# Kernel tuning notes

Measured on AMD Instinct MI355X. Metric: run time of the kernel, lower is better.

The kernel has to match this reference:

```python
import jax, jax.numpy as jnp
import numpy as np

N_NODES = 100000
N_EDGES = 1600000
D = 128


def setup_inputs() -> dict:
    key = jax.random.key(0)
    k1, k2, k3, k4 = jax.random.split(key, 4)
    x = jax.random.normal(k1, (N_NODES, D), dtype=jnp.float32)
    edge_index = jax.random.randint(k2, (2, N_EDGES), 0, N_NODES, dtype=jnp.int32)
    # torch.nn.Linear(nfeat, nclass): weight [out, in], bias [out]
    W = jax.random.normal(k3, (D, D), dtype=jnp.float32) * (1.0 / np.sqrt(D))
    b = jax.random.normal(k4, (D,), dtype=jnp.float32) * 0.01
    return {"x": x, "edge_index": edge_index, "W": W, "b": b}


def reference(x, edge_index, W, b):
    n = x.shape[0]
    # gcn_norm: add self-loops, edge_weight = 1
    loop = jnp.arange(n, dtype=edge_index.dtype)
    row = jnp.concatenate([edge_index[0], loop])  # source
    col = jnp.concatenate([edge_index[1], loop])  # target
    deg = jax.ops.segment_sum(jnp.ones_like(col, dtype=x.dtype), col, num_segments=n)
    dinv = jnp.where(deg > 0, deg ** -0.5, 0.0)
    norm = dinv[row] * dinv[col]  # [E+N]
    # K=1 propagate: out[col] += norm * x[row]
    agg = jax.ops.segment_sum(x[row] * norm[:, None], col, num_segments=n)
    # linear (y = agg @ W^T + b), then relu + residual
    h = agg @ W.T + b
    return x + jax.nn.relu(h)
```

## Files before the change

### kernel.cpp

```cpp
#include <hip/hip_runtime.h>

#define NN 100000
#define NE 1600000
#define DD 128
#define NBLK 98
#define NBUK 782
#define NB_AC 256
#define CHUNK 6250
#define SCAN_N (NBUK * NB_AC)
#define NB_SCAN 196

typedef __attribute__((ext_vector_type(8))) short bf16x8;
typedef __attribute__((ext_vector_type(4))) float f32x4;
typedef __attribute__((ext_vector_type(2))) float f32x2;

__device__ __forceinline__ float bf2f(unsigned short u) {
    return __uint_as_float(((unsigned)u) << 16);
}
__device__ __forceinline__ unsigned short f2bf(float f) {
    unsigned u = __float_as_uint(f);
    u += 0x7FFFu + ((u >> 16) & 1u);
    return (unsigned short)(u >> 16);
}

__global__ __launch_bounds__(256) void k_hist(const int* __restrict__ col,
                                              unsigned* __restrict__ part) {
    __shared__ unsigned hist[NBUK];
    int t = threadIdx.x, blk = blockIdx.x;
    for (int i = t; i < NBUK; i += 256) hist[i] = 0;
    __syncthreads();
    int beg = blk * CHUNK, end = beg + CHUNK;
    for (int e = beg + t; e < end; e += 256)
        atomicAdd(&hist[col[e] >> 7], 1u);
    __syncthreads();
    for (int i = t; i < NBUK; i += 256)
        part[(size_t)i * NB_AC + blk] = hist[i];
}

__global__ __launch_bounds__(1024) void k_bsum(const unsigned* __restrict__ part,
                                               unsigned* __restrict__ sb) {
    __shared__ unsigned red[1024];
    int t = threadIdx.x;
    int i = blockIdx.x * 1024 + t;
    red[t] = i < SCAN_N ? part[i] : 0;
    __syncthreads();
    for (int off = 512; off > 0; off >>= 1) {
        if (t < off) red[t] += red[t + off];
        __syncthreads();
    }
    if (t == 0) sb[blockIdx.x] = red[0];
}

__global__ __launch_bounds__(1024) void k_scanpart(const unsigned* __restrict__ part,
                                                   const unsigned* __restrict__ sb,
                                                   unsigned* __restrict__ off) {
    __shared__ unsigned s2[256];
    __shared__ unsigned s[1024];
    int t = threadIdx.x;
    if (t < 256) s2[t] = (t < NB_SCAN) ? sb[t] : 0;
    __syncthreads();
    for (int o = 1; o < 256; o <<= 1) {
        unsigned v = 0;
        if (t < 256 && t >= o) v = s2[t - o];
        __syncthreads();
        if (t < 256) s2[t] += v;
        __syncthreads();
    }
    unsigned boff = blockIdx.x == 0 ? 0 : s2[blockIdx.x - 1];
    int i = blockIdx.x * 1024 + t;
    unsigned v = i < SCAN_N ? part[i] : 0;
    s[t] = v;
    __syncthreads();
    for (int o = 1; o < 1024; o <<= 1) {
        unsigned u = t >= o ? s[t - o] : 0;
        __syncthreads();
        s[t] += u;
        __syncthreads();
    }
    if (i < SCAN_N) off[i] = boff + s[t] - v;
}

__global__ __launch_bounds__(256) void k_scatter_pk(const int* __restrict__ row,
                                                    const int* __restrict__ col,
                                                    const unsigned* __restrict__ off,
                                                    unsigned* __restrict__ packed) {
    __shared__ unsigned cur[NBUK];
    int t = threadIdx.x, blk = blockIdx.x;
    for (int i = t; i < NBUK; i += 256) cur[i] = off[(size_t)i * NB_AC + blk];
    __syncthreads();
    int beg = blk * CHUNK, end = beg + CHUNK;
    for (int e = beg + t; e < end; e += 256) {
        int c = col[e];
        unsigned pos = atomicAdd(&cur[c >> 7], 1u);
        packed[pos] = ((unsigned)(c & 127) << 17) | (unsigned)row[e];
    }
}

__global__ __launch_bounds__(256) void k_bucket_csr(const unsigned* __restrict__ off,
                                                    const unsigned* __restrict__ packed,
                                                    float* __restrict__ dinv,
                                                    int* __restrict__ rowptr,
                                                    int* __restrict__ esrc) {
    __shared__ unsigned deg[128], pre[128], tmp[128];
    int t = threadIdx.x;
    int buk = blockIdx.x;
    unsigned bstart = off[(size_t)buk * NB_AC];
    unsigned bend = (buk == NBUK - 1) ? (unsigned)NE : off[(size_t)(buk + 1) * NB_AC];
    if (t < 128) deg[t] = 0;
    __syncthreads();
    for (unsigned e = bstart + t; e < bend; e += 256)
        atomicAdd(&deg[packed[e] >> 17], 1u);
    __syncthreads();
    if (t < 128) tmp[t] = deg[t];
    __syncthreads();
    for (int o = 1; o < 128; o <<= 1) {
        unsigned v = 0;
        if (t < 128 && t >= o) v = tmp[t - o];
        __syncthreads();
        if (t < 128) tmp[t] += v;
        __syncthreads();
    }
    if (t < 128) {
        pre[t] = tmp[t] - deg[t];
        int n = buk * 128 + t;
        if (n < NN) {
            dinv[n] = 1.0f / sqrtf((float)(deg[t] + 1));
            rowptr[n] = (int)(bstart + pre[t]);
        }
    }
    if (buk == NBUK - 1 && t == 0) rowptr[NN] = NE;
    __syncthreads();
    if (t < 128) deg[t] = pre[t];
    __syncthreads();
    for (unsigned e = bstart + t; e < bend; e += 256) {
        unsigned p = packed[e];
        unsigned pos = atomicAdd(&deg[p >> 17], 1u);
        esrc[bstart + pos] = (int)(p & 0x1FFFFu);
    }
}

__global__ void k_wb(const float* __restrict__ W, unsigned short* __restrict__ wbs) {
    int unit = blockIdx.x * 256 + threadIdx.x;
    int row = unit >> 4;
    int c0 = (unit & 15) * 8;
    float4 v0 = *(const float4*)(W + row * DD + c0);
    float4 v1 = *(const float4*)(W + row * DD + c0 + 4);
    bf16x8 h;
    h[0] = (short)f2bf(v0.x); h[1] = (short)f2bf(v0.y);
    h[2] = (short)f2bf(v0.z); h[3] = (short)f2bf(v0.w);
    h[4] = (short)f2bf(v1.x); h[5] = (short)f2bf(v1.y);
    h[6] = (short)f2bf(v1.z); h[7] = (short)f2bf(v1.w);
    int byte = (row * 256 + c0 * 2) ^ ((row & 7) << 4);
    *(bf16x8*)((char*)wbs + byte) = h;
}

__global__ __launch_bounds__(256) void k_ygemm(const float* __restrict__ x,
                                               const unsigned short* __restrict__ wbs,
                                               const float* __restrict__ dinv,
                                               unsigned char* __restrict__ yb8) {
    __shared__ unsigned short wb[DD * DD];
    int t = threadIdx.x;
#pragma unroll
    for (int i = 0; i < 8; ++i)
        ((float4*)wb)[t + 256 * i] = ((const float4*)wbs)[t + 256 * i];
    __syncthreads();

    int wave = t >> 6;
    int lane = t & 63;
    int lrow = lane & 15;
    int kg = lane >> 4;

    int arow = blockIdx.x * 64 + wave * 16 + lrow;
    int arc = arow < NN ? arow : NN - 1;
    bf16x8 afrag[4];
#pragma unroll
    for (int ks = 0; ks < 4; ++ks) {
        const float* src = x + (size_t)arc * DD + ks * 32 + kg * 8;
        float4 v0 = *(const float4*)src;
        float4 v1 = *(const float4*)(src + 4);
        bf16x8 h;
        h[0] = (short)f2bf(v0.x); h[1] = (short)f2bf(v0.y);
        h[2] = (short)f2bf(v0.z); h[3] = (short)f2bf(v0.w);
        h[4] = (short)f2bf(v1.x); h[5] = (short)f2bf(v1.y);
        h[6] = (short)f2bf(v1.z); h[7] = (short)f2bf(v1.w);
        afrag[ks] = h;
    }

    f32x4 acc[8];
#pragma unroll
    for (int ct = 0; ct < 8; ++ct) acc[ct] = (f32x4)(0.f);

#pragma unroll
    for (int ct = 0; ct < 8; ++ct) {
        int wrow = ct * 16 + lrow;
#pragma unroll
        for (int ks = 0; ks < 4; ++ks) {
            int byte = (wrow * 256 + ks * 64 + kg * 16) ^ ((wrow & 7) << 4);
            bf16x8 bfrag = *(const bf16x8*)((char*)wb + byte);
            acc[ct] = __builtin_amdgcn_mfma_f32_16x16x32_bf16(afrag[ks], bfrag, acc[ct], 0, 0, 0);
        }
    }

#pragma unroll
    for (int j = 0; j < 4; ++j) {
        int m = blockIdx.x * 64 + wave * 16 + kg * 4 + j;
        if (m < NN) {
            float s = dinv[m];
            unsigned w0 = 0, w1 = 0;
            w0 = __builtin_amdgcn_cvt_pk_fp8_f32(s * acc[0][j], s * acc[1][j], w0, false);
            w0 = __builtin_amdgcn_cvt_pk_fp8_f32(s * acc[2][j], s * acc[3][j], w0, true);
            w1 = __builtin_amdgcn_cvt_pk_fp8_f32(s * acc[4][j], s * acc[5][j], w1, false);
            w1 = __builtin_amdgcn_cvt_pk_fp8_f32(s * acc[6][j], s * acc[7][j], w1, true);
            uint2 o; o.x = w0; o.y = w1;
            *(uint2*)(yb8 + (size_t)m * DD + lrow * 8) = o;
        }
    }
}

__global__ __launch_bounds__(256) void k_gather_fp8(const int* __restrict__ rowptr,
                                                    const int* __restrict__ esrc,
                                                    const unsigned char* __restrict__ yb8,
                                                    const float* __restrict__ x,
                                                    const float* __restrict__ dinv,
                                                    const float* __restrict__ bias,
                                                    float* __restrict__ out) {
    int t = threadIdx.x;
    int gl = t & 31;
    int node = blockIdx.x * 8 + (t >> 5);
    if (node >= NN) return;
    int beg = rowptr[node];
    int end = rowptr[node + 1];
    float dc = dinv[node];

    unsigned su = *(const unsigned*)(yb8 + (size_t)node * DD + gl * 4);
    f32x2 a01 = __builtin_amdgcn_cvt_pk_f32_fp8(su, false);
    f32x2 a23 = __builtin_amdgcn_cvt_pk_f32_fp8(su, true);

    int e = beg;
    for (; e + 7 < end; e += 8) {
        unsigned uu[8];
#pragma unroll
        for (int u = 0; u < 8; ++u) {
            int r = esrc[e + u];
            uu[u] = *(const unsigned*)(yb8 + (size_t)r * DD + gl * 4);
        }
#pragma unroll
        for (int u = 0; u < 8; ++u) {
            a01 += __builtin_amdgcn_cvt_pk_f32_fp8(uu[u], false);
            a23 += __builtin_amdgcn_cvt_pk_f32_fp8(uu[u], true);
        }
    }
    for (; e < end; ++e) {
        int r = esrc[e];
        unsigned u = *(const unsigned*)(yb8 + (size_t)r * DD + gl * 4);
        a01 += __builtin_amdgcn_cvt_pk_f32_fp8(u, false);
        a23 += __builtin_amdgcn_cvt_pk_f32_fp8(u, true);
    }

    float vals[4] = {a01.x, a01.y, a23.x, a23.y};
    int q = gl >> 1;
    int c0 = (gl & 1) * 4;
#pragma unroll
    for (int i = 0; i < 4; ++i) {
        int n = (c0 + i) * 16 + q;
        float h = dc * vals[i] + bias[n];
        out[(size_t)node * DD + n] = x[(size_t)node * DD + n] + fmaxf(h, 0.f);
    }
}

__global__ void k_count(const int* __restrict__ col, int* __restrict__ deg) {
    int i = blockIdx.x * blockDim.x + threadIdx.x;
    if (i < NE) atomicAdd(&deg[col[i]], 1);
}
__global__ __launch_bounds__(1024) void k_blocksum_dinv(const int* __restrict__ deg,
                                                        int* __restrict__ bsum,
                                                        float* __restrict__ dinv) {
    __shared__ int red[1024];
    int t = threadIdx.x;
    int i = blockIdx.x * 1024 + t;
    int d = i < NN ? deg[i] : 0;
    if (i < NN) dinv[i] = 1.0f / sqrtf((float)(d + 1));
    red[t] = d;
    __syncthreads();
    for (int off = 512; off > 0; off >>= 1) {
        if (t < off) red[t] += red[t + off];
        __syncthreads();
    }
    if (t == 0) bsum[blockIdx.x] = red[0];
}
__global__ void k_scanbsum(const int* __restrict__ bsum, int* __restrict__ boff) {
    __shared__ int s[128];
    int t = threadIdx.x;
    s[t] = t < NBLK ? bsum[t] : 0;
    __syncthreads();
    for (int off = 1; off < 128; off <<= 1) {
        int v = t >= off ? s[t - off] : 0;
        __syncthreads();
        s[t] += v;
        __syncthreads();
    }
    if (t < NBLK) boff[t] = (t == 0) ? 0 : s[t - 1];
}
__global__ __launch_bounds__(1024) void k_scanwrite(const int* __restrict__ deg,
                                                    const int* __restrict__ boff,
                                                    int* __restrict__ rowptr) {
    __shared__ int s[1024];
    int t = threadIdx.x;
    int i = blockIdx.x * 1024 + t;
    int v = i < NN ? deg[i] : 0;
    s[t] = v;
    __syncthreads();
    for (int off = 1; off < 1024; off <<= 1) {
        int u = t >= off ? s[t - off] : 0;
        __syncthreads();
        s[t] += u;
        __syncthreads();
    }
    if (i < NN) rowptr[i] = boff[blockIdx.x] + s[t] - v;
    if (i == 0) rowptr[NN] = NE;
}
__global__ void k_fill(const int* __restrict__ row, const int* __restrict__ col,
                       const int* __restrict__ rowptr, int* __restrict__ cnt,
                       int* __restrict__ esrc) {
    int i = blockIdx.x * blockDim.x + threadIdx.x;
    if (i < NE) {
        int c = col[i];
        int pos = rowptr[c] + atomicAdd(&cnt[c], 1);
        esrc[pos] = row[i];
    }
}
__global__ __launch_bounds__(256) void k_gather(const int* __restrict__ rowptr,
                                                const int* __restrict__ esrc,
                                                const float* __restrict__ x,
                                                const float* __restrict__ dinv,
                                                float* __restrict__ agg) {
    int t = threadIdx.x;
    int lane = t & 31;
    int node = blockIdx.x * 8 + (t >> 5);
    if (node >= NN) return;
    int beg = rowptr[node];
    int end = rowptr[node + 1];
    float dc = dinv[node];
    float4 xv = ((const float4*)(x + (size_t)node * DD))[lane];
    float4 acc;
    acc.x = dc * xv.x; acc.y = dc * xv.y; acc.z = dc * xv.z; acc.w = dc * xv.w;
    int e = beg;
    for (; e + 1 < end; e += 2) {
        int r0 = esrc[e];
        int r1 = esrc[e + 1];
        float s0 = dinv[r0];
        float s1 = dinv[r1];
        float4 v0 = ((const float4*)(x + (size_t)r0 * DD))[lane];
        float4 v1 = ((const float4*)(x + (size_t)r1 * DD))[lane];
        acc.x += s0 * v0.x + s1 * v1.x;
        acc.y += s0 * v0.y + s1 * v1.y;
        acc.z += s0 * v0.z + s1 * v1.z;
        acc.w += s0 * v0.w + s1 * v1.w;
    }
    if (e < end) {
        int r = esrc[e];
        float s = dinv[r];
        float4 v = ((const float4*)(x + (size_t)r * DD))[lane];
        acc.x += s * v.x; acc.y += s * v.y; acc.z += s * v.z; acc.w += s * v.w;
    }
    acc.x *= dc; acc.y *= dc; acc.z *= dc; acc.w *= dc;
    ((float4*)(agg + (size_t)node * DD))[lane] = acc;
}
__global__ void k_transpose_w(const float* __restrict__ W, float* __restrict__ Wt) {
    int c = blockIdx.x;
    int k = threadIdx.x;
    Wt[k * DD + c] = W[c * DD + k];
}
__global__ __launch_bounds__(256) void k_gemm(const float* __restrict__ x,
                                              const float* __restrict__ Wt,
                                              const float* __restrict__ bias,
                                              float* __restrict__ out) {
    __shared__ float wt[DD * DD];
    int t = threadIdx.x;
    for (int i = t; i < DD * DD / 4; i += 256)
        ((float4*)wt)[i] = ((const float4*)Wt)[i];
    __syncthreads();

    int grp = t >> 5;
    int c4  = (t & 31) * 4;
    int rbase = blockIdx.x * 64 + grp * 8;

    float acc[8][4];
#pragma unroll
    for (int i = 0; i < 8; i++)
#pragma unroll
        for (int j = 0; j < 4; j++) acc[i][j] = 0.0f;

    for (int k = 0; k < DD; k += 4) {
        float4 w0 = *(const float4*)&wt[(k + 0) * DD + c4];
        float4 w1 = *(const float4*)&wt[(k + 1) * DD + c4];
        float4 w2 = *(const float4*)&wt[(k + 2) * DD + c4];
        float4 w3 = *(const float4*)&wt[(k + 3) * DD + c4];
#pragma unroll
        for (int i = 0; i < 8; i++) {
            int rr = rbase + i;
            rr = rr < NN ? rr : NN - 1;
            float4 a = *(const float4*)&out[(size_t)rr * DD + k];
            acc[i][0] += a.x * w0.x + a.y * w1.x + a.z * w2.x + a.w * w3.x;
            acc[i][1] += a.x * w0.y + a.y * w1.y + a.z * w2.y + a.w * w3.y;
            acc[i][2] += a.x * w0.z + a.y * w1.z + a.z * w2.z + a.w * w3.z;
            acc[i][3] += a.x * w0.w + a.y * w1.w + a.z * w2.w + a.w * w3.w;
        }
    }

    float4 bv = *(const float4*)&bias[c4];
#pragma unroll
    for (int i = 0; i < 8; i++) {
        int r = rbase + i;
        if (r < NN) {
            float4 xv = *(const float4*)&x[(size_t)r * DD + c4];
            float4 o;
            o.x = xv.x + fmaxf(acc[i][0] + bv.x, 0.0f);
            o.y = xv.y + fmaxf(acc[i][1] + bv.y, 0.0f);
            o.z = xv.z + fmaxf(acc[i][2] + bv.z, 0.0f);
            o.w = xv.w + fmaxf(acc[i][3] + bv.w, 0.0f);
            *(float4*)&out[(size_t)r * DD + c4] = o;
        }
    }
}

extern "C" void kernel_launch(void* const* d_in, const int* in_sizes, int n_in,
                              void* d_out, int out_size, void* d_ws, size_t ws_size,
                              hipStream_t stream) {
    const float* x   = (const float*)d_in[0];
    const int*   ei  = (const int*)d_in[1];
    const float* W   = (const float*)d_in[2];
    const float* b   = (const float*)d_in[3];
    const int* row = ei;
    const int* col = ei + NE;

    float* out = (float*)d_out;

    char* ws = (char*)d_ws;
    unsigned* part   = (unsigned*)ws;
    unsigned* off    = (unsigned*)(ws + 800768);
    unsigned* sb     = (unsigned*)(ws + 1601536);
    float*    dinv   = (float*)(ws + 1602352);
    int*      rowptr = (int*)(ws + 2002352);
    unsigned* packed = (unsigned*)(ws + 2402368);
    unsigned short* wbs = (unsigned short*)(ws + 8802368);
    float*    Wt     = (float*)(ws + 8802368);
    int*      esrc   = (int*)(ws + 8867904);
    unsigned char* yb8 = (unsigned char*)(ws + 15267904);

    bool big_ws = ws_size >= 28100000;

    if (big_ws) {
        k_hist<<<NB_AC, 256, 0, stream>>>(col, part);
        k_bsum<<<NB_SCAN, 1024, 0, stream>>>(part, sb);
        k_scanpart<<<NB_SCAN, 1024, 0, stream>>>(part, sb, off);
        k_scatter_pk<<<NB_AC, 256, 0, stream>>>(row, col, off, packed);
        k_bucket_csr<<<NBUK, 256, 0, stream>>>(off, packed, dinv, rowptr, esrc);
        k_wb<<<8, 256, 0, stream>>>(W, wbs);
        k_ygemm<<<(NN + 63) / 64, 256, 0, stream>>>(x, wbs, dinv, yb8);
        k_gather_fp8<<<(NN + 7) / 8, 256, 0, stream>>>(rowptr, esrc, yb8, x, dinv, b, out);
    } else {
        int* cnt  = (int*)ws;
        int* bsum = (int*)(ws + 1601536);
        int* boff = (int*)(ws + 400000);
        hipMemsetAsync(cnt, 0, NN * sizeof(int), stream);
        k_count<<<(NE + 255) / 256, 256, 0, stream>>>(col, cnt);
        k_blocksum_dinv<<<NBLK, 1024, 0, stream>>>(cnt, bsum, dinv);
        k_scanbsum<<<1, 128, 0, stream>>>(bsum, boff);
        k_scanwrite<<<NBLK, 1024, 0, stream>>>(cnt, boff, rowptr);
        hipMemsetAsync(cnt, 0, NN * sizeof(int), stream);
        k_fill<<<(NE + 255) / 256, 256, 0, stream>>>(row, col, rowptr, cnt, esrc);
        k_gather<<<(NN + 7) / 8, 256, 0, stream>>>(rowptr, esrc, x, dinv, out);
        k_transpose_w<<<DD, DD, 0, stream>>>(W, Wt);
        k_gemm<<<(NN + 63) / 64, 256, 0, stream>>>(x, Wt, b, out);
    }
}
```

Before: 135.0 us.

## Split fp8 features into column planes and gather in four cache-sized passes

The GEMM now writes its fp8 output as four column planes of 32 bytes per node instead of one 128-byte row per node. The single gather kernel is replaced by four launches, one per plane. Each launch gathers only a 3.2MB plane, with 8 lanes per edge and 4 edges in flight per 32-lane group, then reduces with shuffles. The aim is for each plane's random-access working set to fit in the per-XCD L2. In exchange, rowptr and esrc are re-read four times, there are extra kernel launches, and only a quarter of the lanes do the epilogue.

```diff
diff --git a/kernel.cpp b/kernel.cpp
--- a/kernel.cpp
+++ b/kernel.cpp
@@ -206,65 +206,78 @@
         int m = blockIdx.x * 64 + wave * 16 + kg * 4 + j;
         if (m < NN) {
             float s = dinv[m];
-            unsigned w0 = 0, w1 = 0;
-            w0 = __builtin_amdgcn_cvt_pk_fp8_f32(s * acc[0][j], s * acc[1][j], w0, false);
-            w0 = __builtin_amdgcn_cvt_pk_fp8_f32(s * acc[2][j], s * acc[3][j], w0, true);
-            w1 = __builtin_amdgcn_cvt_pk_fp8_f32(s * acc[4][j], s * acc[5][j], w1, false);
-            w1 = __builtin_amdgcn_cvt_pk_fp8_f32(s * acc[6][j], s * acc[7][j], w1, true);
-            uint2 o; o.x = w0; o.y = w1;
-            *(uint2*)(yb8 + (size_t)m * DD + lrow * 8) = o;
-        }
-    }
-}
-
-__global__ __launch_bounds__(256) void k_gather_fp8(const int* __restrict__ rowptr,
-                                                    const int* __restrict__ esrc,
-                                                    const unsigned char* __restrict__ yb8,
-                                                    const float* __restrict__ x,
-                                                    const float* __restrict__ dinv,
-                                                    const float* __restrict__ bias,
-                                                    float* __restrict__ out) {
-    int t = threadIdx.x;
-    int gl = t & 31;
+#pragma unroll
+            for (int q = 0; q < 4; ++q) {
+                unsigned w = __builtin_amdgcn_cvt_pk_fp8_f32(s * acc[2 * q][j],
+                                                             s * acc[2 * q + 1][j], 0, false);
+                *(unsigned short*)(yb8 + ((size_t)q * NN + m) * 32 + lrow * 2) =
+                    (unsigned short)w;
+            }
+        }
+    }
+}
+
+__global__ __launch_bounds__(256) void k_gpass(const int* __restrict__ rowptr,
+                                               const int* __restrict__ esrc,
+                                               const unsigned char* __restrict__ plane,
+                                               const float* __restrict__ xq,
+                                               const float* __restrict__ dinv,
+                                               const float* __restrict__ biasq,
+                                               float* __restrict__ outq) {
+    int t = threadIdx.x;
     int node = blockIdx.x * 8 + (t >> 5);
     if (node >= NN) return;
+    int l = t & 31;
+    int sub = l >> 3;
+    int d = l & 7;
     int beg = rowptr[node];
     int end = rowptr[node + 1];
-    float dc = dinv[node];
-
-    unsigned su = *(const unsigned*)(yb8 + (size_t)node * DD + gl * 4);
-    f32x2 a01 = __builtin_amdgcn_cvt_pk_f32_fp8(su, false);
-    f32x2 a23 = __builtin_amdgcn_cvt_pk_f32_fp8(su, true);
-
+
+    f32x2 lo = (f32x2)(0.f), hi = (f32x2)(0.f);
     int e = beg;
-    for (; e + 7 < end; e += 8) {
-        unsigned uu[8];
-#pragma unroll
-        for (int u = 0; u < 8; ++u) {
-            int r = esrc[e + u];
-            uu[u] = *(const unsigned*)(yb8 + (size_t)r * DD + gl * 4);
-        }
-#pragma unroll
-        for (int u = 0; u < 8; ++u) {
-            a01 += __builtin_amdgcn_cvt_pk_f32_fp8(uu[u], false);
-            a23 += __builtin_amdgcn_cvt_pk_f32_fp8(uu[u], true);
-        }
-    }
-    for (; e < end; ++e) {
-        int r = esrc[e];
-        unsigned u = *(const unsigned*)(yb8 + (size_t)r * DD + gl * 4);
-        a01 += __builtin_amdgcn_cvt_pk_f32_fp8(u, false);
-        a23 += __builtin_amdgcn_cvt_pk_f32_fp8(u, true);
-    }
-
-    float vals[4] = {a01.x, a01.y, a23.x, a23.y};
-    int q = gl >> 1;
-    int c0 = (gl & 1) * 4;
-#pragma unroll
-    for (int i = 0; i < 4; ++i) {
-        int n = (c0 + i) * 16 + q;
-        float h = dc * vals[i] + bias[n];
-        out[(size_t)node * DD + n] = x[(size_t)node * DD + n] + fmaxf(h, 0.f);
+    for (; e + 8 <= end; e += 8) {
+        int s0 = esrc[e + sub];
+        int s1 = esrc[e + 4 + sub];
+        unsigned v0 = *(const unsigned*)(plane + (size_t)s0 * 32 + d * 4);
+        unsigned v1 = *(const unsigned*)(plane + (size_t)s1 * 32 + d * 4);
+        lo += __builtin_amdgcn_cvt_pk_f32_fp8(v0, false);
+        hi += __builtin_amdgcn_cvt_pk_f32_fp8(v0, true);
+        lo += __builtin_amdgcn_cvt_pk_f32_fp8(v1, false);
+        hi += __builtin_amdgcn_cvt_pk_f32_fp8(v1, true);
+    }
+    for (; e < end; e += 4) {
+        int ee = e + sub;
+        unsigned v = 0;
+        if (ee < end) {
+            int s = esrc[ee];
+            v = *(const unsigned*)(plane + (size_t)s * 32 + d * 4);
+        }
+        lo += __builtin_amdgcn_cvt_pk_f32_fp8(v, false);
+        hi += __builtin_amdgcn_cvt_pk_f32_fp8(v, true);
+    }
+
+    lo.x += __shfl_xor(lo.x, 8);  lo.x += __shfl_xor(lo.x, 16);
+    lo.y += __shfl_xor(lo.y, 8);  lo.y += __shfl_xor(lo.y, 16);
+    hi.x += __shfl_xor(hi.x, 8);  hi.x += __shfl_xor(hi.x, 16);
+    hi.y += __shfl_xor(hi.y, 8);  hi.y += __shfl_xor(hi.y, 16);
+
+    if (sub == 0) {
+        unsigned sv = *(const unsigned*)(plane + (size_t)node * 32 + d * 4);
+        lo += __builtin_amdgcn_cvt_pk_f32_fp8(sv, false);
+        hi += __builtin_amdgcn_cvt_pk_f32_fp8(sv, true);
+
+        float dc = dinv[node];
+        f32x2 ba = *(const f32x2*)(biasq + 2 * d);
+        f32x2 bb = *(const f32x2*)(biasq + 16 + 2 * d);
+        f32x2 xa = __builtin_nontemporal_load((const f32x2*)(xq + (size_t)node * DD + 2 * d));
+        f32x2 xb = __builtin_nontemporal_load((const f32x2*)(xq + (size_t)node * DD + 16 + 2 * d));
+        f32x2 oa, ob;
+        oa.x = xa.x + fmaxf(dc * lo.x + ba.x, 0.f);
+        oa.y = xa.y + fmaxf(dc * hi.x + ba.y, 0.f);
+        ob.x = xb.x + fmaxf(dc * lo.y + bb.x, 0.f);
+        ob.y = xb.y + fmaxf(dc * hi.y + bb.y, 0.f);
+        __builtin_nontemporal_store(oa, (f32x2*)(outq + (size_t)node * DD + 2 * d));
+        __builtin_nontemporal_store(ob, (f32x2*)(outq + (size_t)node * DD + 16 + 2 * d));
     }
 }
 
@@ -458,7 +471,11 @@
         k_bucket_csr<<<NBUK, 256, 0, stream>>>(off, packed, dinv, rowptr, esrc);
         k_wb<<<8, 256, 0, stream>>>(W, wbs);
         k_ygemm<<<(NN + 63) / 64, 256, 0, stream>>>(x, wbs, dinv, yb8);
-        k_gather_fp8<<<(NN + 7) / 8, 256, 0, stream>>>(rowptr, esrc, yb8, x, dinv, b, out);
+        for (int q = 0; q < 4; ++q) {
+            k_gpass<<<(NN + 7) / 8, 256, 0, stream>>>(
+                rowptr, esrc, yb8 + (size_t)q * NN * 32,
+                x + q * 32, dinv, b + q * 32, out + q * 32);
+        }
     } else {
         int* cnt  = (int*)ws;
         int* bsum = (int*)(ws + 1601536);
```

Measured after the change: 181.9 us. +34.7%, slower.
